# Performance work log

Measured on AMD Instinct MI355X. Metric: run time of the kernel, lower is better.

Reference implementation:

```python
import jax, jax.numpy as jnp
import numpy as np
import math

BS, QLEN, DIM, NHEADS = 2, 2048, 1024, 16
DPH = DIM // NHEADS


def setup_inputs() -> dict:
    key = jax.random.key(0)
    ks = jax.random.split(key, 10)
    s = 0.02
    return {
        "input": jax.random.normal(ks[0], (BS, QLEN, DIM), jnp.float32),
        "mask": jax.random.randint(ks[1], (BS, QLEN), 0, 2, jnp.int32),
        "Wq": jax.random.normal(ks[2], (DIM, DIM), jnp.float32) * s,
        "bq": jnp.zeros((DIM,), jnp.float32),
        "Wk": jax.random.normal(ks[3], (DIM, DIM), jnp.float32) * s,
        "bk": jnp.zeros((DIM,), jnp.float32),
        "Wv": jax.random.normal(ks[4], (DIM, DIM), jnp.float32) * s,
        "bv": jnp.zeros((DIM,), jnp.float32),
        "Wo": jax.random.normal(ks[5], (DIM, DIM), jnp.float32) * s,
        "bo": jnp.zeros((DIM,), jnp.float32),
    }


def _shape(x):
    # (bs, len, dim) -> (bs, heads, len, dph)
    return x.reshape(BS, -1, NHEADS, DPH).transpose(0, 2, 1, 3)


def reference(input, mask, Wq, bq, Wk, bk, Wv, bv, Wo, bo):
    q = _shape(input @ Wq.T + bq)
    k = _shape(input @ Wk.T + bk)
    v = _shape(input @ Wv.T + bv)
    q = q / math.sqrt(DPH)
    scores = jnp.einsum("bhqd,bhkd->bhqk", q, k)  # (bs, h, qlen, klen)
    # original masked_fill_ with 1e-10 (NOT -inf)
    m = (mask == 0)[:, None, None, :]  # (bs,1,1,klen)
    scores = jnp.where(m, jnp.float32(1e-10), scores)
    weights = jax.nn.softmax(scores.astype(jnp.float32), axis=-1).astype(scores.dtype)
    # dropout p=0.0 / eval mode -> identity
    context = jnp.einsum("bhqk,bhkd->bhqd", weights, v)
    context = context.transpose(0, 2, 1, 3).reshape(BS, -1, DIM)
    return context @ Wo.T + bo
```

## Files before the change

kernel.cpp:

```cpp
#include <hip/hip_runtime.h>

typedef __attribute__((ext_vector_type(8))) _Float16 half8;
typedef __attribute__((ext_vector_type(4))) _Float16 half4;
typedef __attribute__((ext_vector_type(4))) float f32x4;
typedef __attribute__((ext_vector_type(16))) float f32x16;
typedef __attribute__((ext_vector_type(4))) int int4v;

#define BS 2
#define QLEN 2048
#define DIM 1024
#define NH 16
#define DPH 64
#define MTOT (BS * QLEN)
#define LOG2E 1.44269504088896340736f

#define WAITB(N)                                          \
    asm volatile("s_waitcnt vmcnt(" #N ")" ::: "memory"); \
    __builtin_amdgcn_s_barrier();                         \
    __builtin_amdgcn_sched_barrier(0)
#define ENDB()                                            \
    __builtin_amdgcn_sched_barrier(0);                    \
    __builtin_amdgcn_s_barrier()

__global__ void cvt_all(const float* __restrict__ x,
                        const float* __restrict__ wq, const float* __restrict__ wk,
                        const float* __restrict__ wv, const float* __restrict__ wo,
                        _Float16* __restrict__ X16,
                        _Float16* __restrict__ Wq16, _Float16* __restrict__ Wk16,
                        _Float16* __restrict__ Wv16, _Float16* __restrict__ Wo16) {
    const int NX = (MTOT * DIM) / 4;
    const int NW = (DIM * DIM) / 4;
    const int total = NX + 4 * NW;
    int idx = blockIdx.x * blockDim.x + threadIdx.x;
    int stride = gridDim.x * blockDim.x;
    for (int i = idx; i < total; i += stride) {
        const float* src; _Float16* dst; int off;
        if (i < NX) { src = x; dst = X16; off = i; }
        else {
            int k = i - NX; int which = k / NW; off = k - which * NW;
            src = which == 0 ? wq : which == 1 ? wk : which == 2 ? wv : wo;
            dst = which == 0 ? Wq16 : which == 1 ? Wk16 : which == 2 ? Wv16 : Wo16;
        }
        float4 v = ((const float4*)src)[off];
        half4 o;
        o[0] = (_Float16)v.x; o[1] = (_Float16)v.y;
        o[2] = (_Float16)v.z; o[3] = (_Float16)v.w;
        ((half4*)dst)[off] = o;
    }
}

__device__ __forceinline__ void gload_lds16(const _Float16* g, _Float16* l) {
    __builtin_amdgcn_global_load_lds(
        (const __attribute__((address_space(1))) void*)g,
        (__attribute__((address_space(3))) void*)l, 16, 0, 0);
}

__global__ __launch_bounds__(256) void gemm_qkv(
    const _Float16* __restrict__ A,
    const _Float16* __restrict__ Wq, const _Float16* __restrict__ Wk,
    const _Float16* __restrict__ Wv,
    const float* __restrict__ bq, const float* __restrict__ bk,
    const float* __restrict__ bv, const int* __restrict__ mask,
    _Float16* __restrict__ Qd, _Float16* __restrict__ Kd,
    _Float16* __restrict__ Vd) {
    const int K = 1024;
    __shared__ _Float16 sm[16384];

    const int flat = blockIdx.x;
    const int xcd = flat & 7, seq = flat >> 3;
    const int ya = xcd >> 1, nb = xcd & 1;
    const int n_hi = seq & 3;
    const int rem = seq >> 2;
    const int z = rem % 3, y_hi = rem / 3;
    const int y = y_hi * 4 + ya;
    const int nblk = n_hi * 2 + nb;
    const int m0 = y * 128, n0 = nblk * 128;

    const _Float16* W = (z == 0) ? Wq : (z == 1) ? Wk : Wv;
    const float* bias = (z == 0) ? bq : (z == 1) ? bk : bv;

    const int tid = threadIdx.x, w = tid >> 6, l = tid & 63;
    const int wr = (w >> 1) * 64, wc = (w & 1) * 64;
    const int r = l & 15, g = l >> 4;

    const _Float16* gA[2];
    const _Float16* gW[2];
    _Float16* dA[2];
    _Float16* dB[2];
#pragma unroll
    for (int i = 0; i < 2; ++i) {
        int s = tid + i * 256, row = s >> 2, pos = s & 3;
        int chunk = pos ^ (row & 3);
        gA[i] = &A[(size_t)(m0 + row) * K + chunk * 8];
        gW[i] = &W[(size_t)(n0 + row) * K + chunk * 8];
        dA[i] = &sm[s * 8];
        dB[i] = &sm[8192 + s * 8];
    }
    auto stageAdv = [&](int bb) {
#pragma unroll
        for (int i = 0; i < 2; ++i) {
            gload_lds16(gA[i], dA[i] + bb * 4096);
            gload_lds16(gW[i], dB[i] + bb * 4096);
            gA[i] += 32;
            gW[i] += 32;
        }
    };

    const int fpos = (g ^ (r & 3)) * 8;
    const _Float16* pA[4];
    const _Float16* pB[4];
#pragma unroll
    for (int i = 0; i < 4; ++i) {
        pA[i] = &sm[(wr + i * 16 + r) * 32] + fpos;
        pB[i] = &sm[8192 + (wc + i * 16 + r) * 32] + fpos;
    }

    f32x4 acc[4][4] = {};
    auto compute = [&](int bb) {
        const int boff = bb * 4096;
        half8 af[4], bf[4];
#pragma unroll
        for (int i = 0; i < 4; ++i) {
            af[i] = *(const half8*)(pA[i] + boff);
            bf[i] = *(const half8*)(pB[i] + boff);
        }
#pragma unroll
        for (int i = 0; i < 4; ++i)
#pragma unroll
            for (int j = 0; j < 4; ++j)
                acc[i][j] = __builtin_amdgcn_mfma_f32_16x16x32_f16(
                    af[i], bf[j], acc[i][j], 0, 0, 0);
    };

    stageAdv(0);
    for (int t = 0; t < 16; ++t) {
        stageAdv(1);
        WAITB(4);
        compute(0);
        ENDB();
        stageAdv(0);
        WAITB(4);
        compute(1);
        ENDB();
    }
    asm volatile("s_waitcnt vmcnt(0)" ::: "memory");
    __builtin_amdgcn_s_barrier();

    float bv4[4];
#pragma unroll
    for (int j = 0; j < 4; ++j) bv4[j] = bias[n0 + wc + j * 16 + r];

    if (z != 2) {
#pragma unroll
        for (int i = 0; i < 4; ++i)
#pragma unroll
            for (int j = 0; j < 4; ++j)
#pragma unroll
                for (int reg = 0; reg < 4; ++reg) {
                    const int m = wr + i * 16 + g * 4 + reg;
                    const int n = wc + j * 16 + r;
                    float v = acc[i][j][reg] + bv4[j];
                    if (z == 0) v *= 0.125f * LOG2E;
                    sm[m * 128 + (((n >> 3) ^ (m & 15)) * 8) + (n & 7)] =
                        (_Float16)v;
                }
    } else {
#pragma unroll
        for (int i = 0; i < 4; ++i)
#pragma unroll
            for (int j = 0; j < 4; ++j)
#pragma unroll
                for (int reg = 0; reg < 4; ++reg) {
                    const int m = wr + i * 16 + g * 4 + reg;
                    const int n = wc + j * 16 + r;
                    float v = acc[i][j][reg] + bv4[j];
                    sm[n * 128 + (((m >> 3) ^ (n & 15)) * 8) + (m & 7)] =
                        (_Float16)v;
                }
    }
    __syncthreads();

    const int bb = m0 >> 11;
    if (z != 2) {
        _Float16* dst0 = (z == 0) ? Qd : Kd;
        const half8 zz = {};
#pragma unroll
        for (int k = 0; k < 8; ++k) {
            const int c = tid * 8 + k;
            const int m = c >> 4, cc = c & 15;
            half8 v = *(const half8*)&sm[m * 128 + ((cc ^ (m & 15)) * 8)];
            const int ttl = (m0 + m) & 2047;
            const int h = (n0 >> 6) + (cc >> 3);
            const int d = (cc & 7) * 8;
            if (z == 1 && mask[bb * QLEN + ttl] == 0) v = zz;
            *(half8*)&dst0[(((size_t)(bb * NH + h)) * QLEN + ttl) * DPH + d] = v;
        }
    } else {
#pragma unroll
        for (int k = 0; k < 8; ++k) {
            const int c = tid * 8 + k;
            const int dl = c >> 4, cc = c & 15;
            half8 v = *(const half8*)&sm[dl * 128 + ((cc ^ (dl & 15)) * 8)];
            const int ng = n0 + dl, h = ng >> 6, dg = ng & 63;
            const int tt0 = (m0 & 2047) + cc * 8;
            *(half8*)&Vd[(((size_t)(bb * NH + h)) * DPH + dg) * QLEN + tt0] = v;
        }
    }
}

__global__ __launch_bounds__(256) void gemm_out(
    const _Float16* __restrict__ A, const _Float16* __restrict__ W,
    const float* __restrict__ bias, float* __restrict__ out) {
    const int K = 1024;
    __shared__ _Float16 sA[2][64 * 32];
    __shared__ _Float16 sB[2][128 * 32];
    const int m0 = blockIdx.y * 64, n0 = blockIdx.x * 128;
    const int tid = threadIdx.x, w = tid >> 6, l = tid & 63;
    const int wr = (w >> 1) * 32, wc = (w & 1) * 64;
    const int r = l & 15, g = l >> 4;

    const _Float16* gA;
    const _Float16* gB[2];
    _Float16* dA;
    _Float16* dB[2];
    {
        int s = tid, row = s >> 2, seg = (s & 3) * 8;
        gA = &A[(size_t)(m0 + row) * K + seg];
        dA = &sA[0][s * 8];
    }
#pragma unroll
    for (int i = 0; i < 2; ++i) {
        int s = tid + i * 256, row = s >> 2, seg = (s & 3) * 8;
        gB[i] = &W[(size_t)(n0 + row) * K + seg];
        dB[i] = &sB[0][s * 8];
    }
    auto stageAdv = [&](int bb) {
        gload_lds16(gA, dA + bb * 2048);
        gA += 32;
#pragma unroll
        for (int i = 0; i < 2; ++i) {
            gload_lds16(gB[i], dB[i] + bb * 4096);
            gB[i] += 32;
        }
    };

    const _Float16* pA[2];
    const _Float16* pB[4];
#pragma unroll
    for (int i = 0; i < 2; ++i)
        pA[i] = &sA[0][(wr + i * 16 + r) * 32 + g * 8];
#pragma unroll
    for (int j = 0; j < 4; ++j)
        pB[j] = &sB[0][(wc + j * 16 + r) * 32 + g * 8];

    f32x4 acc[2][4] = {};
    auto compute = [&](int bb) {
        half8 af[2], bf[4];
#pragma unroll
        for (int i = 0; i < 2; ++i)
            af[i] = *(const half8*)(pA[i] + bb * 2048);
#pragma unroll
        for (int j = 0; j < 4; ++j)
            bf[j] = *(const half8*)(pB[j] + bb * 4096);
#pragma unroll
        for (int i = 0; i < 2; ++i)
#pragma unroll
            for (int j = 0; j < 4; ++j)
                acc[i][j] = __builtin_amdgcn_mfma_f32_16x16x32_f16(
                    af[i], bf[j], acc[i][j], 0, 0, 0);
    };

    stageAdv(0);
    for (int t = 0; t < 16; ++t) {
        stageAdv(1);
        WAITB(3);
        compute(0);
        ENDB();
        stageAdv(0);
        WAITB(3);
        compute(1);
        ENDB();
    }

    float bv4[4];
#pragma unroll
    for (int j = 0; j < 4; ++j) bv4[j] = bias[n0 + wc + j * 16 + r];
#pragma unroll
    for (int i = 0; i < 2; ++i)
#pragma unroll
        for (int j = 0; j < 4; ++j) {
            const int n = n0 + wc + j * 16 + r;
#pragma unroll
            for (int reg = 0; reg < 4; ++reg) {
                const int m = m0 + wr + i * 16 + g * 4 + reg;
                out[(size_t)m * DIM + n] = acc[i][j][reg] + bv4[j];
            }
        }
}

__global__ __launch_bounds__(512) void attn_kernel(
    const _Float16* __restrict__ Qg, const _Float16* __restrict__ Kg,
    const _Float16* __restrict__ Vg, _Float16* __restrict__ ctx) {
    __shared__ __align__(16) char smem[65536];

    const int flat = blockIdx.x;
    const int qt = (flat >> 3) & 15;
    const int bh = ((flat >> 7) << 3) | (flat & 7);
    const int b = bh >> 4, h = bh & 15;
    const _Float16* __restrict__ Qp = Qg + (size_t)bh * QLEN * DPH;
    const _Float16* __restrict__ Kp = Kg + (size_t)bh * QLEN * DPH;
    const _Float16* __restrict__ Vp = Vg + (size_t)bh * DPH * QLEN;

    const int tid = threadIdx.x, w = tid >> 6, l = tid & 63;
    const int qsub = w & 3, ksplit = w >> 2;
    const int ln = l & 31, hi = l >> 5;
    const int q0 = qt * 128 + qsub * 32;
    const int kbase = ksplit * 1024;

    _Float16* sK0 = (_Float16*)(smem + ksplit * 2 * 8192);
    _Float16* sV0 = (_Float16*)(smem + 32768 + ksplit * 2 * 8192);

    half8 qf[4];
#pragma unroll
    for (int ks = 0; ks < 4; ++ks)
        qf[ks] = *(const half8*)&Qp[(size_t)(q0 + ln) * DPH + ks * 16 + hi * 8];

    f32x16 accT[2] = {};
    float lsum = 0.f;

    const _Float16* kptr[2][4];
    const _Float16* vptr[2][2][2];
#pragma unroll
    for (int kb = 0; kb < 2; ++kb) {
#pragma unroll
        for (int ks = 0; ks < 4; ++ks)
            kptr[kb][ks] = sK0 + (kb * 32 + ln) * 64 + ((ks * 2 + hi) ^ (ln & 7)) * 8;
#pragma unroll
        for (int dblk = 0; dblk < 2; ++dblk) {
            vptr[kb][dblk][0] =
                sV0 + (dblk * 32 + ln) * 64 + ((kb * 4 + 0 + hi) ^ (ln & 7)) * 8;
            vptr[kb][dblk][1] =
                sV0 + (dblk * 32 + ln) * 64 + ((kb * 4 + 2 + hi) ^ (ln & 7)) * 8;
        }
    }

    const int c8 = ((l & 7) ^ (l >> 3)) * 8;
    const int rl = l >> 3;
    const _Float16* gK[2];
    const _Float16* gV[2];
    _Float16* dK[2];
    _Float16* dV[2];
#pragma unroll
    for (int j = 0; j < 2; ++j) {
        const int r0 = qsub * 16 + j * 8;
        gK[j] = &Kp[(size_t)(kbase + r0 + rl) * DPH + c8];
        gV[j] = &Vp[(size_t)(r0 + rl) * QLEN + kbase + c8];
        dK[j] = sK0 + r0 * 64 + l * 8;
        dV[j] = sV0 + r0 * 64 + l * 8;
    }

    auto stageAdv = [&](int bb) {
#pragma unroll
        for (int j = 0; j < 2; ++j) {
            gload_lds16(gK[j], dK[j] + bb * 4096);
            gload_lds16(gV[j], dV[j] + bb * 4096);
            gK[j] += 64 * DPH;
            gV[j] += 64;
        }
    };

    auto compute = [&](int bb) {
        const int boff = bb * 4096;
#pragma unroll
        for (int kb = 0; kb < 2; ++kb) {
            f32x16 st = {};
            __builtin_amdgcn_s_setprio(1);
#pragma unroll
            for (int ks = 0; ks < 4; ++ks) {
                half8 kf = *(const half8*)(kptr[kb][ks] + boff);
                st = __builtin_amdgcn_mfma_f32_32x32x16_f16(kf, qf[ks], st, 0, 0, 0);
            }
            __builtin_amdgcn_s_setprio(0);

            int cpk[8];
#pragma unroll
            for (int i = 0; i < 8; ++i) {
                float e0 = __builtin_amdgcn_exp2f(st[2 * i]);
                float e1 = __builtin_amdgcn_exp2f(st[2 * i + 1]);
                lsum += e0 + e1;
                cpk[i] =
                    __builtin_bit_cast(int, __builtin_amdgcn_cvt_pkrtz(e0, e1));
            }
            asm("v_permlane32_swap_b32 %0, %1" : "+v"(cpk[0]), "+v"(cpk[2]));
            asm("v_permlane32_swap_b32 %0, %1" : "+v"(cpk[1]), "+v"(cpk[3]));
            asm("v_permlane32_swap_b32 %0, %1" : "+v"(cpk[4]), "+v"(cpk[6]));
            asm("v_permlane32_swap_b32 %0, %1" : "+v"(cpk[5]), "+v"(cpk[7]));
            int4v b0 = {cpk[0], cpk[1], cpk[2], cpk[3]};
            int4v b1 = {cpk[4], cpk[5], cpk[6], cpk[7]};
            half8 Bf0 = __builtin_bit_cast(half8, b0);
            half8 Bf1 = __builtin_bit_cast(half8, b1);

            __builtin_amdgcn_s_setprio(1);
#pragma unroll
            for (int dblk = 0; dblk < 2; ++dblk) {
                half8 vf0 = *(const half8*)(vptr[kb][dblk][0] + boff);
                half8 vf1 = *(const half8*)(vptr[kb][dblk][1] + boff);
                accT[dblk] = __builtin_amdgcn_mfma_f32_32x32x16_f16(
                    vf0, Bf0, accT[dblk], 0, 0, 0);
                accT[dblk] = __builtin_amdgcn_mfma_f32_32x32x16_f16(
                    vf1, Bf1, accT[dblk], 0, 0, 0);
            }
            __builtin_amdgcn_s_setprio(0);
        }
    };

    stageAdv(0);
    for (int t = 0; t < 8; ++t) {
        stageAdv(1);
        WAITB(4);
        compute(0);
        ENDB();
        stageAdv(0);
        WAITB(4);
        compute(1);
        ENDB();
    }
    asm volatile("s_waitcnt vmcnt(0)" ::: "memory");
    __builtin_amdgcn_s_barrier();

    lsum += __shfl_xor(lsum, 32);

    float* sRed = (float*)smem;
    if (ksplit == 1) {
        float* p = sRed + (qsub * 64 + l) * 33;
#pragma unroll
        for (int dblk = 0; dblk < 2; ++dblk)
#pragma unroll
            for (int i = 0; i < 16; ++i)
                p[dblk * 16 + i] = accT[dblk][i];
        p[32] = lsum;
    }
    __syncthreads();
    if (ksplit == 1) return;

    const float* p = sRed + (qsub * 64 + l) * 33;
#pragma unroll
    for (int dblk = 0; dblk < 2; ++dblk)
#pragma unroll
        for (int i = 0; i < 16; ++i)
            accT[dblk][i] += p[dblk * 16 + i];
    lsum += p[32];

    const float inv = 1.f / lsum;
    _Float16* cp = ctx + ((size_t)(b * QLEN) + q0 + ln) * DIM + h * DPH;
#pragma unroll
    for (int dblk = 0; dblk < 2; ++dblk)
#pragma unroll
        for (int j = 0; j < 4; ++j) {
            half4 o4;
#pragma unroll
            for (int e = 0; e < 4; ++e)
                o4[e] = (_Float16)(accT[dblk][4 * j + e] * inv);
            *(half4*)&cp[dblk * 32 + 8 * j + 4 * hi] = o4;
        }
}

extern "C" void kernel_launch(void* const* d_in, const int* in_sizes, int n_in,
                              void* d_out, int out_size, void* d_ws, size_t ws_size,
                              hipStream_t stream) {
    const float* x  = (const float*)d_in[0];
    const int* mask = (const int*)d_in[1];
    const float* Wq = (const float*)d_in[2];
    const float* bq = (const float*)d_in[3];
    const float* Wk = (const float*)d_in[4];
    const float* bk = (const float*)d_in[5];
    const float* Wv = (const float*)d_in[6];
    const float* bv = (const float*)d_in[7];
    const float* Wo = (const float*)d_in[8];
    const float* bo = (const float*)d_in[9];
    float* out = (float*)d_out;

    char* ws = (char*)d_ws;
    const size_t MB = 1u << 20;
    _Float16* X16  = (_Float16*)(ws + 0);
    _Float16* Wq16 = (_Float16*)(ws + 8 * MB);
    _Float16* Wk16 = (_Float16*)(ws + 10 * MB);
    _Float16* Wv16 = (_Float16*)(ws + 12 * MB);
    _Float16* Wo16 = (_Float16*)(ws + 14 * MB);
    _Float16* Q16  = (_Float16*)(ws + 16 * MB);
    _Float16* K16  = (_Float16*)(ws + 24 * MB);
    _Float16* V16T = (_Float16*)(ws + 32 * MB);
    _Float16* CTX  = (_Float16*)(ws + 40 * MB);

    cvt_all<<<2048, 256, 0, stream>>>(x, Wq, Wk, Wv, Wo,
                                      X16, Wq16, Wk16, Wv16, Wo16);

    gemm_qkv<<<768, 256, 0, stream>>>(
        X16, Wq16, Wk16, Wv16, bq, bk, bv, mask, Q16, K16, V16T);

    attn_kernel<<<512, 512, 0, stream>>>(Q16, K16, V16T, CTX);

    gemm_out<<<dim3(8, 64), 256, 0, stream>>>(CTX, Wo16, bo, out);
}
```

Baseline: 114.1 us.

## Shrink QKV GEMM tile to 64x128 and drop XCD-aware block remapping

The QKV projection GEMM moves from 128x128 tiles on 768 blocks to 64x128 tiles on a 3D grid of 1536 blocks, with a smaller LDS footprint. It also removes the XCD-aware block index swizzle and the XOR swizzle on the LDS staging layout, so fragments are read from plain row-major LDS. The aim is more blocks and better occupancy and load balance. In exchange, arithmetic intensity per tile drops, L2 locality from the swizzled scheduling is lost, and unswizzled LDS reads may hit bank conflicts.

New measurement: 124.6 us. 9.2% more time.

```diff
diff --git a/kernel.cpp b/kernel.cpp
--- a/kernel.cpp
+++ b/kernel.cpp
@@ -64,68 +64,62 @@
     _Float16* __restrict__ Qd, _Float16* __restrict__ Kd,
     _Float16* __restrict__ Vd) {
     const int K = 1024;
-    __shared__ _Float16 sm[16384];
-
-    const int flat = blockIdx.x;
-    const int xcd = flat & 7, seq = flat >> 3;
-    const int ya = xcd >> 1, nb = xcd & 1;
-    const int n_hi = seq & 3;
-    const int rem = seq >> 2;
-    const int z = rem % 3, y_hi = rem / 3;
-    const int y = y_hi * 4 + ya;
-    const int nblk = n_hi * 2 + nb;
-    const int m0 = y * 128, n0 = nblk * 128;
-
+    __shared__ _Float16 sm[12288];
+
+    const int z = blockIdx.z;
+    const int m0 = blockIdx.y * 64, n0 = blockIdx.x * 128;
     const _Float16* W = (z == 0) ? Wq : (z == 1) ? Wk : Wv;
     const float* bias = (z == 0) ? bq : (z == 1) ? bk : bv;
 
     const int tid = threadIdx.x, w = tid >> 6, l = tid & 63;
-    const int wr = (w >> 1) * 64, wc = (w & 1) * 64;
+    const int wr = (w >> 1) * 32, wc = (w & 1) * 64;
     const int r = l & 15, g = l >> 4;
 
-    const _Float16* gA[2];
-    const _Float16* gW[2];
-    _Float16* dA[2];
+    const _Float16* gA;
+    const _Float16* gB[2];
+    _Float16* dA;
     _Float16* dB[2];
+    {
+        int s = tid, row = s >> 2, seg = (s & 3) * 8;
+        gA = &A[(size_t)(m0 + row) * K + seg];
+        dA = &sm[s * 8];
+    }
 #pragma unroll
     for (int i = 0; i < 2; ++i) {
-        int s = tid + i * 256, row = s >> 2, pos = s & 3;
-        int chunk = pos ^ (row & 3);
-        gA[i] = &A[(size_t)(m0 + row) * K + chunk * 8];
-        gW[i] = &W[(size_t)(n0 + row) * K + chunk * 8];
-        dA[i] = &sm[s * 8];
-        dB[i] = &sm[8192 + s * 8];
+        int s = tid + i * 256, row = s >> 2, seg = (s & 3) * 8;
+        gB[i] = &W[(size_t)(n0 + row) * K + seg];
+        dB[i] = &sm[4096 + s * 8];
     }
     auto stageAdv = [&](int bb) {
+        gload_lds16(gA, dA + bb * 2048);
+        gA += 32;
 #pragma unroll
         for (int i = 0; i < 2; ++i) {
-            gload_lds16(gA[i], dA[i] + bb * 4096);
-            gload_lds16(gW[i], dB[i] + bb * 4096);
-            gA[i] += 32;
-            gW[i] += 32;
-        }
-    };
-
-    const int fpos = (g ^ (r & 3)) * 8;
-    const _Float16* pA[4];
+            gload_lds16(gB[i], dB[i] + bb * 4096);
+            gB[i] += 32;
+        }
+    };
+
+    const _Float16* pA[2];
     const _Float16* pB[4];
 #pragma unroll
-    for (int i = 0; i < 4; ++i) {
-        pA[i] = &sm[(wr + i * 16 + r) * 32] + fpos;
-        pB[i] = &sm[8192 + (wc + i * 16 + r) * 32] + fpos;
-    }
-
-    f32x4 acc[4][4] = {};
+    for (int i = 0; i < 2; ++i)
+        pA[i] = &sm[(wr + i * 16 + r) * 32 + g * 8];
+#pragma unroll
+    for (int j = 0; j < 4; ++j)
+        pB[j] = &sm[4096 + (wc + j * 16 + r) * 32 + g * 8];
+
+    f32x4 acc[2][4] = {};
     auto compute = [&](int bb) {
-        const int boff = bb * 4096;
-        half8 af[4], bf[4];
-#pragma unroll
-        for (int i = 0; i < 4; ++i) {
-            af[i] = *(const half8*)(pA[i] + boff);
-            bf[i] = *(const half8*)(pB[i] + boff);
-        }
-#pragma unroll
-        for (int i = 0; i < 4; ++i)
+        half8 af[2], bf[4];
+#pragma unroll
+        for (int i = 0; i < 2; ++i)
+            af[i] = *(const half8*)(pA[i] + bb * 2048);
+#pragma unroll
+        for (int j = 0; j < 4; ++j)
+            bf[j] = *(const half8*)(pB[j] + bb * 4096);
+#pragma unroll
+        for (int i = 0; i < 2; ++i)
 #pragma unroll
             for (int j = 0; j < 4; ++j)
                 acc[i][j] = __builtin_amdgcn_mfma_f32_16x16x32_f16(
@@ -135,11 +129,11 @@
     stageAdv(0);
     for (int t = 0; t < 16; ++t) {
         stageAdv(1);
-        WAITB(4);
+        WAITB(3);
         compute(0);
         ENDB();
         stageAdv(0);
-        WAITB(4);
+        WAITB(3);
         compute(1);
         ENDB();
     }
@@ -152,7 +146,7 @@
 
     if (z != 2) {
 #pragma unroll
-        for (int i = 0; i < 4; ++i)
+        for (int i = 0; i < 2; ++i)
 #pragma unroll
             for (int j = 0; j < 4; ++j)
 #pragma unroll
@@ -166,7 +160,7 @@
                 }
     } else {
 #pragma unroll
-        for (int i = 0; i < 4; ++i)
+        for (int i = 0; i < 2; ++i)
 #pragma unroll
             for (int j = 0; j < 4; ++j)
 #pragma unroll
@@ -174,7 +168,7 @@
                     const int m = wr + i * 16 + g * 4 + reg;
                     const int n = wc + j * 16 + r;
                     float v = acc[i][j][reg] + bv4[j];
-                    sm[n * 128 + (((m >> 3) ^ (n & 15)) * 8) + (m & 7)] =
+                    sm[n * 64 + (((m >> 3) ^ (n & 7)) * 8) + (m & 7)] =
                         (_Float16)v;
                 }
     }
@@ -185,8 +179,8 @@
         _Float16* dst0 = (z == 0) ? Qd : Kd;
         const half8 zz = {};
 #pragma unroll
-        for (int k = 0; k < 8; ++k) {
-            const int c = tid * 8 + k;
+        for (int k = 0; k < 4; ++k) {
+            const int c = tid * 4 + k;
             const int m = c >> 4, cc = c & 15;
             half8 v = *(const half8*)&sm[m * 128 + ((cc ^ (m & 15)) * 8)];
             const int ttl = (m0 + m) & 2047;
@@ -197,10 +191,10 @@
         }
     } else {
 #pragma unroll
-        for (int k = 0; k < 8; ++k) {
-            const int c = tid * 8 + k;
-            const int dl = c >> 4, cc = c & 15;
-            half8 v = *(const half8*)&sm[dl * 128 + ((cc ^ (dl & 15)) * 8)];
+        for (int k = 0; k < 4; ++k) {
+            const int c = tid * 4 + k;
+            const int dl = c >> 3, cc = c & 7;
+            half8 v = *(const half8*)&sm[dl * 64 + ((cc ^ (dl & 7)) * 8)];
             const int ng = n0 + dl, h = ng >> 6, dg = ng & 63;
             const int tt0 = (m0 & 2047) + cc * 8;
             *(half8*)&Vd[(((size_t)(bb * NH + h)) * DPH + dg) * QLEN + tt0] = v;
@@ -495,7 +489,7 @@
     cvt_all<<<2048, 256, 0, stream>>>(x, Wq, Wk, Wv, Wo,
                                       X16, Wq16, Wk16, Wv16, Wo16);
 
-    gemm_qkv<<<768, 256, 0, stream>>>(
+    gemm_qkv<<<dim3(8, 64, 3), 256, 0, stream>>>(
         X16, Wq16, Wk16, Wv16, bq, bk, bv, mask, Q16, K16, V16T);
 
     attn_kernel<<<512, 512, 0, stream>>>(Q16, K16, V16T, CTX);
```
